# Performance work log

Hardware: AMD Instinct MI355X
Metric: run time of the kernel (lower is better)

Reference implementation:

```python
import jax, jax.numpy as jnp
import numpy as np

NCLASS = 19


def setup_inputs() -> dict:
    key = jax.random.key(0)
    k1, k2 = jax.random.split(key)
    logits = jax.random.normal(k1, (4, NCLASS, 512, 1024), dtype=jnp.float32)
    target = jax.random.randint(k2, (4, 512, 1024), 0, NCLASS, dtype=jnp.int32)
    return {"logits": logits, "target": target}


def reference(logits, target):
    # Faithful to the torch module: per predicted class cls,
    #   cls_vectors    = logits values at all (c, pixel) positions whose
    #                    argmax-predicted class == cls, grouped per sample n
    #   cls_prototype  = scalar mean of those values per sample
    #   cls_center_loss = mean_n || cls_vectors_n - prototype_n ||_2
    # and the total loss sums over classes. The Python loop + boolean masked
    # select is replaced by one fused segmented reduction using the identity
    #   sum((x - m)^2) = S2 - S1^2 / K   with m = S1/K.
    N, C, H, W = logits.shape
    probs = jax.nn.softmax(logits, axis=1)
    preds = jnp.argmax(probs, axis=1)              # (N, H, W) int

    x = logits.reshape(N, C, H * W)
    s1 = jnp.sum(x, axis=1).reshape(-1)            # (N*HW,) sum over channels per pixel
    s2 = jnp.sum(x * x, axis=1).reshape(-1)        # (N*HW,)
    ones = jnp.ones_like(s1)

    # segment id = sample index * C + predicted class  -> N*C segments
    seg = (preds.reshape(N, -1) + jnp.arange(N, dtype=preds.dtype)[:, None] * C).reshape(-1)
    data = jnp.stack([s1, s2, ones], axis=-1)      # (N*HW, 3)
    sums = jax.ops.segment_sum(data, seg, num_segments=N * C)  # (N*C, 3)
    sums = sums.reshape(N, C, 3)
    S1, S2, cnt = sums[..., 0], sums[..., 1], sums[..., 2]      # (N, nclass)

    # each matching pixel contributes C values => K = cnt * C elements per (n, cls)
    K = jnp.maximum(cnt, 1.0) * C
    sq_dev = jnp.maximum(S2 - S1 * S1 / K, 0.0)    # sum of squared deviations
    norms = jnp.where(cnt > 0, jnp.sqrt(sq_dev), 0.0)           # (N, nclass)

    center_loss = jnp.sum(jnp.mean(norms, axis=0))  # sum over classes of mean over N
    return center_loss
```

## Files before the change

### kernel.cpp

```cpp
#include <hip/hip_runtime.h>

#define NCLS 19
#define NSMP 4
#define HW   (512 * 1024)
#define NSEG (NSMP * NCLS)

__global__ __launch_bounds__(256) void cl_main(const float* __restrict__ logits,
                                               float* __restrict__ ws) {
    __shared__ float sb[3 * NCLS];
    const int tid = threadIdx.x;
    if (tid < 3 * NCLS) sb[tid] = 0.0f;
    __syncthreads();

    const int    n    = blockIdx.x >> 7;
    const size_t bpix = (size_t)(blockIdx.x & 127) * 4096;
    const float* base = logits + (size_t)n * NCLS * HW + bpix + (size_t)tid * 4;

    #pragma unroll
    for (int r = 0; r < 4; ++r) {
        float4 v[NCLS];
        #pragma unroll
        for (int c = 0; c < NCLS; ++c) {
            v[c] = *(const float4*)(base + (size_t)c * HW + (size_t)r * 1024);
        }
        asm volatile("" ::: "memory");

        float s1[4], s2[4], mv[4];
        int   mi[4];
        {
            const float a0[4] = {v[0].x, v[0].y, v[0].z, v[0].w};
            #pragma unroll
            for (int j = 0; j < 4; ++j) {
                s1[j] = a0[j];
                s2[j] = a0[j] * a0[j];
                mv[j] = a0[j];
                mi[j] = 0;
            }
        }
        #pragma unroll
        for (int c = 1; c < NCLS; ++c) {
            const float a[4] = {v[c].x, v[c].y, v[c].z, v[c].w};
            #pragma unroll
            for (int j = 0; j < 4; ++j) {
                s1[j] += a[j];
                s2[j]  = fmaf(a[j], a[j], s2[j]);
                if (a[j] > mv[j]) { mv[j] = a[j]; mi[j] = c; }
            }
        }

        #pragma unroll
        for (int j = 0; j < 4; ++j) {
            atomicAdd(&sb[mi[j]],      s1[j]);
            atomicAdd(&sb[19 + mi[j]], s2[j]);
            atomicAdd(&sb[38 + mi[j]], 1.0f);
        }
        asm volatile("" ::: "memory");
    }
    __syncthreads();

    if (tid < NCLS) {
        const int seg = n * NCLS + tid;
        atomicAdd(&ws[seg],            sb[tid]);
        atomicAdd(&ws[NSEG + seg],     sb[19 + tid]);
        atomicAdd(&ws[2 * NSEG + seg], sb[38 + tid]);
    }
}

__global__ void cl_final(const float* __restrict__ ws, float* __restrict__ out) {
    __shared__ float red[128];
    const int i = threadIdx.x;
    float v = 0.0f;
    if (i < NSEG) {
        const float S1  = ws[i];
        const float S2  = ws[NSEG + i];
        const float cnt = ws[2 * NSEG + i];
        const float K   = fmaxf(cnt, 1.0f) * (float)NCLS;
        const float sq  = fmaxf(S2 - S1 * S1 / K, 0.0f);
        v = (cnt > 0.0f) ? sqrtf(sq) : 0.0f;
    }
    red[i] = v;
    __syncthreads();
    #pragma unroll
    for (int s = 64; s > 0; s >>= 1) {
        if (i < s) red[i] += red[i + s];
        __syncthreads();
    }
    if (i == 0) out[0] = red[0] / (float)NSMP;
}

extern "C" void kernel_launch(void* const* d_in, const int* in_sizes, int n_in,
                              void* d_out, int out_size, void* d_ws, size_t ws_size,
                              hipStream_t stream) {
    const float* logits = (const float*)d_in[0];
    float* ws  = (float*)d_ws;
    float* out = (float*)d_out;

    hipMemsetAsync(ws, 0, 3 * NSEG * sizeof(float), stream);
    cl_main<<<512, 256, 0, stream>>>(logits, ws);
    cl_final<<<1, 128, 0, stream>>>(ws, out);
}
```

Baseline: 54.65 us.

## Restructure main loop to double-buffer channel loads across all four rows

The loop now iterates over channels on the outside and keeps 16 pixels of running state per thread. Loads for the next channel (four float4 rows) are issued into a second register buffer while the current channel is processed, replacing the old scheme that loaded all 19 channels for one row before computing. The goal is fewer registers in flight per step and overlap of memory latency with compute, which could raise occupancy. The catch is fewer outstanding loads per thread (8 versus 19 float4) and more accumulator state, so memory-level parallelism may drop.

```diff
diff --git a/kernel.cpp b/kernel.cpp
--- a/kernel.cpp
+++ b/kernel.cpp
@@ -16,45 +16,67 @@
     const size_t bpix = (size_t)(blockIdx.x & 127) * 4096;
     const float* base = logits + (size_t)n * NCLS * HW + bpix + (size_t)tid * 4;
 
+    float s1[16], s2[16], mv[16];
+    int   mi[16];
+
+    float4 va[4], vb[4];
     #pragma unroll
-    for (int r = 0; r < 4; ++r) {
-        float4 v[NCLS];
-        #pragma unroll
-        for (int c = 0; c < NCLS; ++c) {
-            v[c] = *(const float4*)(base + (size_t)c * HW + (size_t)r * 1024);
-        }
-        asm volatile("" ::: "memory");
+    for (int r = 0; r < 4; ++r)
+        va[r] = *(const float4*)(base + (size_t)r * 1024);
 
-        float s1[4], s2[4], mv[4];
-        int   mi[4];
-        {
-            const float a0[4] = {v[0].x, v[0].y, v[0].z, v[0].w};
-            #pragma unroll
-            for (int j = 0; j < 4; ++j) {
-                s1[j] = a0[j];
-                s2[j] = a0[j] * a0[j];
-                mv[j] = a0[j];
-                mi[j] = 0;
-            }
-        }
-        #pragma unroll
-        for (int c = 1; c < NCLS; ++c) {
-            const float a[4] = {v[c].x, v[c].y, v[c].z, v[c].w};
-            #pragma unroll
-            for (int j = 0; j < 4; ++j) {
-                s1[j] += a[j];
-                s2[j]  = fmaf(a[j], a[j], s2[j]);
-                if (a[j] > mv[j]) { mv[j] = a[j]; mi[j] = c; }
-            }
-        }
+#define STEPC(CUR, NXT, C, DOLOAD)                                             \
+    do {                                                                       \
+        if (DOLOAD) {                                                          \
+            _Pragma("unroll")                                                  \
+            for (int r = 0; r < 4; ++r)                                        \
+                NXT[r] = *(const float4*)(base + (size_t)((C) + 1) * HW +      \
+                                          (size_t)r * 1024);                   \
+        }                                                                      \
+        _Pragma("unroll")                                                      \
+        for (int r = 0; r < 4; ++r) {                                          \
+            const float a[4] = {CUR[r].x, CUR[r].y, CUR[r].z, CUR[r].w};       \
+            _Pragma("unroll")                                                  \
+            for (int j = 0; j < 4; ++j) {                                      \
+                const int jj = r * 4 + j;           \
+                if ((C) == 0) {                                                \
+                    s1[jj] = a[j]; s2[jj] = a[j] * a[j];                       \
+                    mv[jj] = a[j]; mi[jj] = 0;                                 \
+                } else {                                                       \
+                    s1[jj] += a[j];                                            \
+                    s2[jj]  = fmaf(a[j], a[j], s2[jj]);                        \
+                    if (a[j] > mv[jj]) { mv[jj] = a[j]; mi[jj] = (C); }        \
+                }                                                              \
+            }                                                                  \
+        }                                                                      \
+        asm volatile("" ::: "memory");         \
+    } while (0)
 
-        #pragma unroll
-        for (int j = 0; j < 4; ++j) {
-            atomicAdd(&sb[mi[j]],      s1[j]);
-            atomicAdd(&sb[19 + mi[j]], s2[j]);
-            atomicAdd(&sb[38 + mi[j]], 1.0f);
-        }
-        asm volatile("" ::: "memory");
+    STEPC(va, vb,  0, true);
+    STEPC(vb, va,  1, true);
+    STEPC(va, vb,  2, true);
+    STEPC(vb, va,  3, true);
+    STEPC(va, vb,  4, true);
+    STEPC(vb, va,  5, true);
+    STEPC(va, vb,  6, true);
+    STEPC(vb, va,  7, true);
+    STEPC(va, vb,  8, true);
+    STEPC(vb, va,  9, true);
+    STEPC(va, vb, 10, true);
+    STEPC(vb, va, 11, true);
+    STEPC(va, vb, 12, true);
+    STEPC(vb, va, 13, true);
+    STEPC(va, vb, 14, true);
+    STEPC(vb, va, 15, true);
+    STEPC(va, vb, 16, true);
+    STEPC(vb, va, 17, true);
+    STEPC(va, vb, 18, false);
+#undef STEPC
+
+    #pragma unroll
+    for (int j = 0; j < 16; ++j) {
+        atomicAdd(&sb[mi[j]],      s1[j]);
+        atomicAdd(&sb[19 + mi[j]], s2[j]);
+        atomicAdd(&sb[38 + mi[j]], 1.0f);
     }
     __syncthreads();
 
```

Result: slower. 65.21 us (+19.3%).
